# Kernel tuning notes

Measured on AMD Instinct MI355X. Metric: run time of the kernel, lower is better.

## Reference

```python
import jax, jax.numpy as jnp
import numpy as np

E = 64          # num_experts
D_IN = 512      # in_features
D_OUT = 512     # out_features
T = 262144      # total routed token-slots (grouped by expert, balanced)


def setup_inputs() -> dict:
    key = jax.random.key(0)
    k1, k2 = jax.random.split(key)
    STD = 0.02
    return {
        "input": jax.random.normal(k1, (T, D_IN), dtype=jnp.float32),
        # tokens are pre-grouped by expert; balanced routing -> equal counts
        "num_experts_per_token": jnp.full((E,), T // E, dtype=jnp.int64),
        "weight": jax.random.normal(k2, (E, D_OUT, D_IN), dtype=jnp.float32) * STD,
        "bias": jnp.zeros((E, D_OUT), dtype=jnp.float32),
    }


def reference(input, num_experts_per_token, weight, bias):
    # Faithful to the split + per-expert F.linear + cat path, for balanced
    # routing (equal counts per expert) so shapes are static under jit.
    e = weight.shape[0]
    tpe = input.shape[0] // e  # tokens per expert
    x = input.reshape(e, tpe, -1)                      # [E, tpe, D_in]
    # F.linear(x_e, W_e) = x_e @ W_e.T for each expert -> grouped GEMM
    out = jnp.einsum('eti,eoi->eto', x, weight)        # [E, tpe, D_out]
    out = out + bias[:, None, :]
    return out.reshape(e * tpe, -1)                    # [T, D_out]
```

## Files before the change

### kernel.cpp

```cpp
#include <hip/hip_runtime.h>
#include <hip/hip_bf16.h>


#define NEXPERT 64
#define DIN 512
#define DOUT 512
#define TPE 4096
#define BM 128
#define BN 128
#define BK 32
#define NKT 16

typedef __attribute__((ext_vector_type(8))) __bf16 bf16x8;
typedef __attribute__((ext_vector_type(4))) float f32x4;

__global__ __launch_bounds__(256)
void pack_w_kernel(const float* __restrict__ w, __bf16* __restrict__ wp) {
  int S = blockIdx.x * 256 + threadIdx.x;
  int l  = S & 63;
  int j  = (S >> 6) & 7;
  int kt = (S >> 9) & 15;
  int nt = (S >> 13) & 3;
  int e  = S >> 15;
  int o  = nt * 128 + j * 16 + (l >> 2);
  int kg = (l & 3) ^ ((l >> 3) & 3);
  const float* src = w + ((size_t)(e * DOUT + o)) * DIN + kt * BK + kg * 8;
  f32x4 lo = *(const f32x4*)(src);
  f32x4 hi = *(const f32x4*)(src + 4);
  bf16x8 r;
  r[0]=(__bf16)lo[0]; r[1]=(__bf16)lo[1]; r[2]=(__bf16)lo[2]; r[3]=(__bf16)lo[3];
  r[4]=(__bf16)hi[0]; r[5]=(__bf16)hi[1]; r[6]=(__bf16)hi[2]; r[7]=(__bf16)hi[3];
  *(bf16x8*)(wp + (size_t)S * 8) = r;
}

__global__ __launch_bounds__(256, 3)
void moe_gemm128(const float* __restrict__ x, const __bf16* __restrict__ wp,
                 const float* __restrict__ bias, float* __restrict__ out) {
  __shared__ __align__(16) unsigned char sA[2][BM * BK * 2];
  __shared__ __align__(16) unsigned char sB[2][BN * BK * 2];

  int bid  = blockIdx.x;
  int swzb = (bid & 7) * 1024 + (bid >> 3);
  int e  = swzb >> 7;
  int rr = swzb & 127;
  int mt = rr >> 2;
  int nt = rr & 3;

  const int tid  = threadIdx.x;
  const int lane = tid & 63;
  const int wv   = tid >> 6;
  const int wm   = wv >> 1;
  const int wn   = wv & 1;
  const int r15  = lane & 15;
  const int kg   = lane >> 4;

  const int chz = (kg ^ ((r15 >> 1) & 3)) << 4;
  const int aRd = (wm * 64 + r15) * 64 + chz;
  const int bRd = (wn * 64 + r15) * 64 + chz;

  const int ar = tid >> 1;
  const int h  = tid & 1;
  const float* aG = x + ((size_t)e * TPE + (size_t)mt * BM + ar) * DIN + h * 16;
  const int awB = ar * 64;

  const __bf16* bS0 = wp + (size_t)(e * 4 + nt) * 65536
                         + (size_t)(wv * 2) * 512 + (size_t)lane * 8;

  f32x4 sa0[4], sa1[4];

#define GLOADB(kt, dbuf)                                                     \
  { _Pragma("unroll") for (int i = 0; i < 2; ++i)                            \
      __builtin_amdgcn_global_load_lds(                                      \
          (const __attribute__((address_space(1))) void*)(bS0 +              \
              (size_t)(kt) * 4096 + i * 512),                                \
          (__attribute__((address_space(3))) void*)(&sB[dbuf][(wv * 2 + i) * 1024]), \
          16, 0, 0); }

#define ISSUEA(kt, Sr)                                                       \
  { _Pragma("unroll") for (int i = 0; i < 4; ++i)                            \
      Sr[i] = *(const f32x4*)(aG + (kt) * BK + i * 4); }

#define WRITEA(dbuf, Sr)                                                     \
  { _Pragma("unroll") for (int i = 0; i < 2; ++i) {                          \
      bf16x8 cc;                                                             \
      cc[0]=(__bf16)Sr[i*2][0];   cc[1]=(__bf16)Sr[i*2][1];                  \
      cc[2]=(__bf16)Sr[i*2][2];   cc[3]=(__bf16)Sr[i*2][3];                  \
      cc[4]=(__bf16)Sr[i*2+1][0]; cc[5]=(__bf16)Sr[i*2+1][1];                \
      cc[6]=(__bf16)Sr[i*2+1][2]; cc[7]=(__bf16)Sr[i*2+1][3];                \
      *(bf16x8*)(&sA[dbuf][awB + (((h*2+i) ^ ((ar >> 1) & 3)) << 4)]) = cc; } }

  f32x4 acc[4][4];
#pragma unroll
  for (int m = 0; m < 4; ++m)
#pragma unroll
    for (int n = 0; n < 4; ++n) acc[m][n] = (f32x4)0.f;

  GLOADB(0, 0);
  ISSUEA(0, sa0);
  ISSUEA(1, sa1);
  WRITEA(0, sa0);
  asm volatile("s_waitcnt lgkmcnt(0)" ::: "memory");
  __builtin_amdgcn_s_barrier();

#pragma unroll
  for (int t = 0; t < NKT; ++t) {
    const int d = t & 1;
    if (t == NKT - 1) {
      asm volatile("s_waitcnt vmcnt(0)" ::: "memory");
    } else {
      asm volatile("s_waitcnt vmcnt(4)" ::: "memory");
    }
    if (t + 1 < NKT) GLOADB(t + 1, d ^ 1);
    bf16x8 bfr[4], af[4];
#pragma unroll
    for (int ni = 0; ni < 4; ++ni)
      bfr[ni] = *(const bf16x8*)(&sB[d][bRd + ni * 1024]);
#pragma unroll
    for (int mi = 0; mi < 4; ++mi)
      af[mi] = *(const bf16x8*)(&sA[d][aRd + mi * 1024]);

    if (t + 2 < NKT) {
      if (d == 0) { ISSUEA(t + 2, sa0); } else { ISSUEA(t + 2, sa1); }
    }
    __builtin_amdgcn_s_setprio(1);
#pragma unroll
    for (int mi = 0; mi < 2; ++mi)
#pragma unroll
      for (int ni = 0; ni < 4; ++ni)
        acc[mi][ni] = __builtin_amdgcn_mfma_f32_16x16x32_bf16(
            af[mi], bfr[ni], acc[mi][ni], 0, 0, 0);
    __builtin_amdgcn_s_setprio(0);

    if (t + 1 < NKT) {
      if (d == 0) { WRITEA(1, sa1); } else { WRITEA(0, sa0); }
    }

    __builtin_amdgcn_s_setprio(1);
#pragma unroll
    for (int mi = 2; mi < 4; ++mi)
#pragma unroll
      for (int ni = 0; ni < 4; ++ni)
        acc[mi][ni] = __builtin_amdgcn_mfma_f32_16x16x32_bf16(
            af[mi], bfr[ni], acc[mi][ni], 0, 0, 0);
    __builtin_amdgcn_s_setprio(0);

    if (t + 1 < NKT) {
      asm volatile("s_waitcnt lgkmcnt(0)" ::: "memory");
      __builtin_amdgcn_s_barrier();
    }
  }

  float bv[4];
  const float* bp = bias + (size_t)e * DOUT + nt * BN + wn * 64 + r15;
#pragma unroll
  for (int n = 0; n < 4; ++n) bv[n] = bp[n * 16];

  const int q4 = (lane >> 4) * 4;
  float* Cb = out + ((size_t)e * TPE + (size_t)mt * BM + wm * 64) * DOUT
              + nt * BN + wn * 64;
#pragma unroll
  for (int m = 0; m < 4; ++m) {
#pragma unroll
    for (int j = 0; j < 4; ++j) {
      float* pr = Cb + (size_t)(m * 16 + q4 + j) * DOUT;
#pragma unroll
      for (int n = 0; n < 4; ++n)
        pr[n * 16 + r15] = acc[m][n][j] + bv[n];
    }
  }
#undef GLOADB
#undef ISSUEA
#undef WRITEA
}

__device__ __forceinline__ bf16x8 cvt8f(f32x4 lo, f32x4 hi) {
  bf16x8 r;
  r[0]=(__bf16)lo[0]; r[1]=(__bf16)lo[1]; r[2]=(__bf16)lo[2]; r[3]=(__bf16)lo[3];
  r[4]=(__bf16)hi[0]; r[5]=(__bf16)hi[1]; r[6]=(__bf16)hi[2]; r[7]=(__bf16)hi[3];
  return r;
}

__global__ __launch_bounds__(256)
void moe_fallback(const float* __restrict__ x, const float* __restrict__ w,
                  const float* __restrict__ bias, float* __restrict__ out) {
  __shared__ bf16x8 fA[2][512];
  __shared__ bf16x8 fB[2][512];
  int bid = blockIdx.x;
  int swz = (bid & 7) * 1024 + (bid >> 3);
  int e = swz >> 7, rr = swz & 127, mt = rr >> 2, nt = rr & 3;
  const int t = threadIdx.x, lane = t & 63, wave = t >> 6;
  const int wm = wave >> 1, wnn = wave & 1, r15 = lane & 15, kgf = lane >> 4;
  const int rs = r15 * 4 + (kgf ^ ((r15 >> 1) & 3));
  const int row0 = t >> 2, kg0 = t & 3;
  const int slot0 = row0 * 4 + (kg0 ^ ((row0 >> 1) & 3));
  const int slot1 = slot0 + 256;
  const float* Ab = x + ((size_t)e * TPE + (size_t)mt * 128) * DIN;
  const float* Bb = w + ((size_t)e * DOUT + (size_t)nt * 128) * DIN;
  const int offA0 = row0 * DIN + kg0 * 8, offA1 = offA0 + 64 * DIN;
  f32x4 a0l, a0h, a1l, a1h, b0l, b0h, b1l, b1h;
  auto LOAD = [&](int kt) {
    const float* pa0 = Ab + offA0 + kt * 32; const float* pa1 = Ab + offA1 + kt * 32;
    const float* pb0 = Bb + offA0 + kt * 32; const float* pb1 = Bb + offA1 + kt * 32;
    a0l = *(const f32x4*)(pa0); a0h = *(const f32x4*)(pa0 + 4);
    a1l = *(const f32x4*)(pa1); a1h = *(const f32x4*)(pa1 + 4);
    b0l = *(const f32x4*)(pb0); b0h = *(const f32x4*)(pb0 + 4);
    b1l = *(const f32x4*)(pb1); b1h = *(const f32x4*)(pb1 + 4);
  };
  auto STORE = [&](int buf) {
    fA[buf][slot0] = cvt8f(a0l, a0h); fA[buf][slot1] = cvt8f(a1l, a1h);
    fB[buf][slot0] = cvt8f(b0l, b0h); fB[buf][slot1] = cvt8f(b1l, b1h);
  };
  f32x4 acc[4][4];
#pragma unroll
  for (int m = 0; m < 4; ++m)
#pragma unroll
    for (int n = 0; n < 4; ++n) acc[m][n] = (f32x4)0.f;
  LOAD(0); STORE(0); __syncthreads();
  int cur = 0;
  for (int kt = 0; kt < 16; ++kt) {
    if (kt + 1 < 16) LOAD(kt + 1);
    bf16x8 af[4], bfr[4];
#pragma unroll
    for (int m = 0; m < 4; ++m) af[m] = fA[cur][wm * 256 + m * 64 + rs];
#pragma unroll
    for (int n = 0; n < 4; ++n) bfr[n] = fB[cur][wnn * 256 + n * 64 + rs];
#pragma unroll
    for (int m = 0; m < 4; ++m)
#pragma unroll
      for (int n = 0; n < 4; ++n)
        acc[m][n] = __builtin_amdgcn_mfma_f32_16x16x32_bf16(af[m], bfr[n], acc[m][n], 0, 0, 0);
    if (kt + 1 < 16) { STORE(cur ^ 1); __syncthreads(); }
    cur ^= 1;
  }
  float bv[4];
  const float* bp = bias + (size_t)e * DOUT + nt * 128 + wnn * 64 + r15;
#pragma unroll
  for (int n = 0; n < 4; ++n) bv[n] = bp[n * 16];
  const int q4 = (lane >> 4) * 4;
  float* Cb = out + ((size_t)e * TPE + (size_t)mt * 128 + wm * 64) * DOUT + nt * 128 + wnn * 64;
#pragma unroll
  for (int m = 0; m < 4; ++m)
#pragma unroll
    for (int j = 0; j < 4; ++j) {
      float* pr = Cb + (size_t)(m * 16 + q4 + j) * DOUT;
#pragma unroll
      for (int n = 0; n < 4; ++n) pr[n * 16 + r15] = acc[m][n][j] + bv[n];
    }
}

extern "C" void kernel_launch(void* const* d_in, const int* in_sizes, int n_in,
                              void* d_out, int out_size, void* d_ws, size_t ws_size,
                              hipStream_t stream) {
  const float* x    = (const float*)d_in[0];
  const float* w    = (const float*)d_in[2];
  const float* bias = (const float*)d_in[3];
  float* out        = (float*)d_out;

  const size_t wElems = (size_t)NEXPERT * DOUT * DIN;
  const size_t needWs = wElems * sizeof(__hip_bfloat16);

  if (ws_size >= needWs) {
    dim3 pgrid(wElems / 8 / 256);
    hipLaunchKernelGGL(pack_w_kernel, pgrid, dim3(256), 0, stream,
                       w, (__bf16*)d_ws);
    dim3 grid(NEXPERT * (TPE / BM) * (DOUT / BN));
    hipLaunchKernelGGL(moe_gemm128, grid, dim3(256), 0, stream,
                       x, (const __bf16*)d_ws, bias, out);
  } else {
    dim3 grid(NEXPERT * 32 * 4);
    hipLaunchKernelGGL(moe_fallback, grid, dim3(256), 0, stream, x, w, bias, out);
  }
}
```

Measured before the change: 359.2 us.

## Drop LDS staging; load MFMA fragments directly from global memory

Replaces the LDS double-buffered grouped GEMM with a kernel where each wave loads its A fragments (fp32, converted to bf16 in registers) and B fragments straight from global memory. The weight pack kernel now writes bf16 weights in per-lane MFMA fragment order, so each B load is one contiguous 16-byte vector per lane. The loop is software-pipelined over two k-steps with register double buffering. This removes LDS writes and reads and all block barriers. In exchange, A and B tiles are fetched redundantly by the two waves that share them, which relies on L1/L2 hits, and more registers are live.

```diff
diff --git a/kernel.cpp b/kernel.cpp
--- a/kernel.cpp
+++ b/kernel.cpp
@@ -6,45 +6,42 @@
 #define DIN 512
 #define DOUT 512
 #define TPE 4096
-#define BM 128
-#define BN 128
-#define BK 32
 #define NKT 16
 
 typedef __attribute__((ext_vector_type(8))) __bf16 bf16x8;
 typedef __attribute__((ext_vector_type(4))) float f32x4;
 
-__global__ __launch_bounds__(256)
-void pack_w_kernel(const float* __restrict__ w, __bf16* __restrict__ wp) {
-  int S = blockIdx.x * 256 + threadIdx.x;
-  int l  = S & 63;
-  int j  = (S >> 6) & 7;
-  int kt = (S >> 9) & 15;
-  int nt = (S >> 13) & 3;
-  int e  = S >> 15;
-  int o  = nt * 128 + j * 16 + (l >> 2);
-  int kg = (l & 3) ^ ((l >> 3) & 3);
-  const float* src = w + ((size_t)(e * DOUT + o)) * DIN + kt * BK + kg * 8;
-  f32x4 lo = *(const f32x4*)(src);
-  f32x4 hi = *(const f32x4*)(src + 4);
+__device__ __forceinline__ bf16x8 cvt8(f32x4 lo, f32x4 hi) {
   bf16x8 r;
   r[0]=(__bf16)lo[0]; r[1]=(__bf16)lo[1]; r[2]=(__bf16)lo[2]; r[3]=(__bf16)lo[3];
   r[4]=(__bf16)hi[0]; r[5]=(__bf16)hi[1]; r[6]=(__bf16)hi[2]; r[7]=(__bf16)hi[3];
-  *(bf16x8*)(wp + (size_t)S * 8) = r;
+  return r;
+}
+
+__global__ __launch_bounds__(256)
+void pack_w_frag(const float* __restrict__ w, __bf16* __restrict__ wp) {
+  int S  = blockIdx.x * 256 + threadIdx.x;
+  int l  = S & 63;
+  int kt = (S >> 6) & 15;
+  int ng = (S >> 10) & 31;
+  int e  = S >> 15;
+  int o  = ng * 16 + (l & 15);
+  int k  = kt * 32 + (l >> 4) * 8;
+  const float* src = w + ((size_t)(e * DOUT + o)) * DIN + k;
+  f32x4 lo = *(const f32x4*)src;
+  f32x4 hi = *(const f32x4*)(src + 4);
+  *(bf16x8*)(wp + (size_t)S * 8) = cvt8(lo, hi);
 }
 
 __global__ __launch_bounds__(256, 3)
-void moe_gemm128(const float* __restrict__ x, const __bf16* __restrict__ wp,
-                 const float* __restrict__ bias, float* __restrict__ out) {
-  __shared__ __align__(16) unsigned char sA[2][BM * BK * 2];
-  __shared__ __align__(16) unsigned char sB[2][BN * BK * 2];
-
+void moe_nolds(const float* __restrict__ x, const __bf16* __restrict__ wp,
+               const float* __restrict__ bias, float* __restrict__ out) {
   int bid  = blockIdx.x;
   int swzb = (bid & 7) * 1024 + (bid >> 3);
-  int e  = swzb >> 7;
-  int rr = swzb & 127;
-  int mt = rr >> 2;
-  int nt = rr & 3;
+  int e   = swzb >> 7;
+  int rr  = swzb & 127;
+  int mt  = rr >> 2;
+  int nt2 = rr & 3;
 
   const int tid  = threadIdx.x;
   const int lane = tid & 63;
@@ -54,40 +51,34 @@
   const int r15  = lane & 15;
   const int kg   = lane >> 4;
 
-  const int chz = (kg ^ ((r15 >> 1) & 3)) << 4;
-  const int aRd = (wm * 64 + r15) * 64 + chz;
-  const int bRd = (wn * 64 + r15) * 64 + chz;
-
-  const int ar = tid >> 1;
-  const int h  = tid & 1;
-  const float* aG = x + ((size_t)e * TPE + (size_t)mt * BM + ar) * DIN + h * 16;
-  const int awB = ar * 64;
-
-  const __bf16* bS0 = wp + (size_t)(e * 4 + nt) * 65536
-                         + (size_t)(wv * 2) * 512 + (size_t)lane * 8;
-
-  f32x4 sa0[4], sa1[4];
-
-#define GLOADB(kt, dbuf)                                                     \
-  { _Pragma("unroll") for (int i = 0; i < 2; ++i)                            \
-      __builtin_amdgcn_global_load_lds(                                      \
-          (const __attribute__((address_space(1))) void*)(bS0 +              \
-              (size_t)(kt) * 4096 + i * 512),                                \
-          (__attribute__((address_space(3))) void*)(&sB[dbuf][(wv * 2 + i) * 1024]), \
-          16, 0, 0); }
-
-#define ISSUEA(kt, Sr)                                                       \
-  { _Pragma("unroll") for (int i = 0; i < 4; ++i)                            \
-      Sr[i] = *(const f32x4*)(aG + (kt) * BK + i * 4); }
-
-#define WRITEA(dbuf, Sr)                                                     \
-  { _Pragma("unroll") for (int i = 0; i < 2; ++i) {                          \
-      bf16x8 cc;                                                             \
-      cc[0]=(__bf16)Sr[i*2][0];   cc[1]=(__bf16)Sr[i*2][1];                  \
-      cc[2]=(__bf16)Sr[i*2][2];   cc[3]=(__bf16)Sr[i*2][3];                  \
-      cc[4]=(__bf16)Sr[i*2+1][0]; cc[5]=(__bf16)Sr[i*2+1][1];                \
-      cc[6]=(__bf16)Sr[i*2+1][2]; cc[7]=(__bf16)Sr[i*2+1][3];                \
-      *(bf16x8*)(&sA[dbuf][awB + (((h*2+i) ^ ((ar >> 1) & 3)) << 4)]) = cc; } }
+  const float* aB = x + ((size_t)e * TPE + mt * 128 + wm * 64 + r15) * DIN + kg * 8;
+  const __bf16* bB = wp + (((size_t)(e * 32 + nt2 * 8 + wn * 4) * 16) * 64
+                           + (size_t)lane) * 8;
+
+  f32x4  at[8];
+  bf16x8 af[4];
+  bf16x8 bfr0[4], bfr1[4];
+
+#define LOADA(kt)                                                            \
+  { _Pragma("unroll") for (int i = 0; i < 8; ++i)                            \
+      at[i] = *(const f32x4*)(aB + (size_t)(i >> 1) * 16 * DIN               \
+                               + (kt) * 32 + (i & 1) * 4); }
+
+#define LOADB(kt, Bv)                                                        \
+  { _Pragma("unroll") for (int ni = 0; ni < 4; ++ni)                         \
+      Bv[ni] = *(const bf16x8*)(bB + ni * 8192 + (kt) * 512); }
+
+#define CVTA()                                                               \
+  { _Pragma("unroll") for (int mi = 0; mi < 4; ++mi)                         \
+      af[mi] = cvt8(at[mi * 2], at[mi * 2 + 1]); }
+
+#define MFMAS(Bv)                                                            \
+  { __builtin_amdgcn_s_setprio(1);                                           \
+    _Pragma("unroll") for (int mi = 0; mi < 4; ++mi)                         \
+      _Pragma("unroll") for (int ni = 0; ni < 4; ++ni)                       \
+        acc[mi][ni] = __builtin_amdgcn_mfma_f32_16x16x32_bf16(               \
+            af[mi], Bv[ni], acc[mi][ni], 0, 0, 0);                           \
+    __builtin_amdgcn_s_setprio(0); }
 
   f32x4 acc[4][4];
 #pragma unroll
@@ -95,69 +86,32 @@
 #pragma unroll
     for (int n = 0; n < 4; ++n) acc[m][n] = (f32x4)0.f;
 
-  GLOADB(0, 0);
-  ISSUEA(0, sa0);
-  ISSUEA(1, sa1);
-  WRITEA(0, sa0);
-  asm volatile("s_waitcnt lgkmcnt(0)" ::: "memory");
-  __builtin_amdgcn_s_barrier();
-
-#pragma unroll
-  for (int t = 0; t < NKT; ++t) {
-    const int d = t & 1;
-    if (t == NKT - 1) {
-      asm volatile("s_waitcnt vmcnt(0)" ::: "memory");
-    } else {
-      asm volatile("s_waitcnt vmcnt(4)" ::: "memory");
+  LOADA(0);
+  LOADB(0, bfr0);
+
+#pragma unroll
+  for (int t2 = 0; t2 < 8; ++t2) {
+    const int kt = t2 * 2;
+    CVTA();
+    LOADA(kt + 1);
+    LOADB(kt + 1, bfr1);
+    MFMAS(bfr0);
+    CVTA();
+    if (kt + 2 < NKT) {
+      LOADA(kt + 2);
+      LOADB(kt + 2, bfr0);
     }
-    if (t + 1 < NKT) GLOADB(t + 1, d ^ 1);
-    bf16x8 bfr[4], af[4];
-#pragma unroll
-    for (int ni = 0; ni < 4; ++ni)
-      bfr[ni] = *(const bf16x8*)(&sB[d][bRd + ni * 1024]);
-#pragma unroll
-    for (int mi = 0; mi < 4; ++mi)
-      af[mi] = *(const bf16x8*)(&sA[d][aRd + mi * 1024]);
-
-    if (t + 2 < NKT) {
-      if (d == 0) { ISSUEA(t + 2, sa0); } else { ISSUEA(t + 2, sa1); }
-    }
-    __builtin_amdgcn_s_setprio(1);
-#pragma unroll
-    for (int mi = 0; mi < 2; ++mi)
-#pragma unroll
-      for (int ni = 0; ni < 4; ++ni)
-        acc[mi][ni] = __builtin_amdgcn_mfma_f32_16x16x32_bf16(
-            af[mi], bfr[ni], acc[mi][ni], 0, 0, 0);
-    __builtin_amdgcn_s_setprio(0);
-
-    if (t + 1 < NKT) {
-      if (d == 0) { WRITEA(1, sa1); } else { WRITEA(0, sa0); }
-    }
-
-    __builtin_amdgcn_s_setprio(1);
-#pragma unroll
-    for (int mi = 2; mi < 4; ++mi)
-#pragma unroll
-      for (int ni = 0; ni < 4; ++ni)
-        acc[mi][ni] = __builtin_amdgcn_mfma_f32_16x16x32_bf16(
-            af[mi], bfr[ni], acc[mi][ni], 0, 0, 0);
-    __builtin_amdgcn_s_setprio(0);
-
-    if (t + 1 < NKT) {
-      asm volatile("s_waitcnt lgkmcnt(0)" ::: "memory");
-      __builtin_amdgcn_s_barrier();
-    }
+    MFMAS(bfr1);
   }
 
   float bv[4];
-  const float* bp = bias + (size_t)e * DOUT + nt * BN + wn * 64 + r15;
+  const float* bp = bias + (size_t)e * DOUT + nt2 * 128 + wn * 64 + r15;
 #pragma unroll
   for (int n = 0; n < 4; ++n) bv[n] = bp[n * 16];
 
   const int q4 = (lane >> 4) * 4;
-  float* Cb = out + ((size_t)e * TPE + (size_t)mt * BM + wm * 64) * DOUT
-              + nt * BN + wn * 64;
+  float* Cb = out + ((size_t)e * TPE + mt * 128 + wm * 64) * DOUT
+              + nt2 * 128 + wn * 64;
 #pragma unroll
   for (int m = 0; m < 4; ++m) {
 #pragma unroll
@@ -168,17 +122,13 @@
         pr[n * 16 + r15] = acc[m][n][j] + bv[n];
     }
   }
-#undef GLOADB
-#undef ISSUEA
-#undef WRITEA
-}
-
-__device__ __forceinline__ bf16x8 cvt8f(f32x4 lo, f32x4 hi) {
-  bf16x8 r;
-  r[0]=(__bf16)lo[0]; r[1]=(__bf16)lo[1]; r[2]=(__bf16)lo[2]; r[3]=(__bf16)lo[3];
-  r[4]=(__bf16)hi[0]; r[5]=(__bf16)hi[1]; r[6]=(__bf16)hi[2]; r[7]=(__bf16)hi[3];
-  return r;
-}
+#undef LOADA
+#undef LOADB
+#undef CVTA
+#undef MFMAS
+}
+
+typedef __attribute__((ext_vector_type(8))) __bf16 bf16x8f;
 
 __global__ __launch_bounds__(256)
 void moe_fallback(const float* __restrict__ x, const float* __restrict__ w,
@@ -207,8 +157,8 @@
     b1l = *(const f32x4*)(pb1); b1h = *(const f32x4*)(pb1 + 4);
   };
   auto STORE = [&](int buf) {
-    fA[buf][slot0] = cvt8f(a0l, a0h); fA[buf][slot1] = cvt8f(a1l, a1h);
-    fB[buf][slot0] = cvt8f(b0l, b0h); fB[buf][slot1] = cvt8f(b1l, b1h);
+    fA[buf][slot0] = cvt8(a0l, a0h); fA[buf][slot1] = cvt8(a1l, a1h);
+    fB[buf][slot0] = cvt8(b0l, b0h); fB[buf][slot1] = cvt8(b1l, b1h);
   };
   f32x4 acc[4][4];
 #pragma unroll
@@ -261,10 +211,10 @@
 
   if (ws_size >= needWs) {
     dim3 pgrid(wElems / 8 / 256);
-    hipLaunchKernelGGL(pack_w_kernel, pgrid, dim3(256), 0, stream,
+    hipLaunchKernelGGL(pack_w_frag, pgrid, dim3(256), 0, stream,
                        w, (__bf16*)d_ws);
-    dim3 grid(NEXPERT * (TPE / BM) * (DOUT / BN));
-    hipLaunchKernelGGL(moe_gemm128, grid, dim3(256), 0, stream,
+    dim3 grid(NEXPERT * 32 * 4);
+    hipLaunchKernelGGL(moe_nolds, grid, dim3(256), 0, stream,
                        x, (const __bf16*)d_ws, bias, out);
   } else {
     dim3 grid(NEXPERT * 32 * 4);
```

Result: slower. 688.1 us (+91.5%).
